# Optimization experiments

Measured on AMD Instinct MI355X. Metric: run time of the kernel, lower is better.

## Reference

```python
import jax, jax.numpy as jnp
from jax import lax
import numpy as np

B, CIN, H, W = 32, 256, 56, 56
BOTTLE, GROWTH = 128, 32
EPS = 1e-5
QMAX = 127.0  # 8-bit symmetric


def _fq(x, scale, qmax=QMAX):
    # fake-quantize with straight-through estimator
    q = jnp.clip(jnp.round(x / scale), -qmax - 1.0, qmax) * scale
    return x + lax.stop_gradient(q - x)


def fake_quant_act(x):
    # per-tensor symmetric 8-bit activation quantization (QuantAct)
    scale = lax.stop_gradient(jnp.max(jnp.abs(x)) / QMAX + 1e-8)
    return _fq(x, scale), scale


def quant_weight_pc(w):
    # per-output-channel symmetric 8-bit weight quantization, w: [O,I,kh,kw]
    scale = lax.stop_gradient(jnp.max(jnp.abs(w), axis=(1, 2, 3)) / QMAX + 1e-8)
    return _fq(w, scale[:, None, None, None]), scale


def conv2d(x, w, pad):
    return lax.conv_general_dilated(
        x, w, window_strides=(1, 1), padding=[(pad, pad), (pad, pad)],
        dimension_numbers=("NCHW", "OIHW", "NCHW"))


def setup_inputs() -> dict:
    key = jax.random.key(0)
    ks = jax.random.split(key, 12)
    return {
        "batch": jax.random.normal(ks[0], (B, CIN, H, W), jnp.float32),
        "input_scaling_factor": jnp.float32(0.05),
        "bn1_gamma": jax.random.uniform(ks[1], (CIN,), jnp.float32, 0.5, 1.5),
        "bn1_beta": jax.random.normal(ks[2], (CIN,), jnp.float32) * 0.1,
        "bn1_mean": jax.random.normal(ks[3], (CIN,), jnp.float32) * 0.1,
        "bn1_var": jax.random.uniform(ks[4], (CIN,), jnp.float32, 0.5, 1.5),
        "conv1_w": jax.random.normal(ks[5], (BOTTLE, CIN, 1, 1), jnp.float32) * 0.05,
        "bn2_gamma": jax.random.uniform(ks[6], (BOTTLE,), jnp.float32, 0.5, 1.5),
        "bn2_beta": jax.random.normal(ks[7], (BOTTLE,), jnp.float32) * 0.1,
        "bn2_mean": jax.random.normal(ks[8], (BOTTLE,), jnp.float32) * 0.1,
        "bn2_var": jax.random.uniform(ks[9], (BOTTLE,), jnp.float32, 0.5, 1.5),
        "conv2_w": jax.random.normal(ks[10], (GROWTH, BOTTLE, 3, 3), jnp.float32) * 0.05,
    }


def reference(batch, input_scaling_factor, bn1_gamma, bn1_beta, bn1_mean,
              bn1_var, conv1_w, bn2_gamma, bn2_beta, bn2_mean, bn2_var,
              conv2_w):
    s_in = input_scaling_factor
    # ---- QuantBn1: BN with fake-quantized folded weight/bias ----
    w1 = bn1_gamma * lax.rsqrt(bn1_var + EPS)            # [CIN]
    b1 = bn1_beta - bn1_mean * w1                        # [CIN]
    s_bn = lax.stop_gradient(jnp.max(jnp.abs(w1)) / QMAX + 1e-8)
    w1q = _fq(w1, s_bn)
    b1q = _fq(b1, s_in * s_bn, qmax=2.0 ** 31)           # bias quantized at s_in*s_w
    x = batch * w1q[None, :, None, None] + b1q[None, :, None, None]
    x = jax.nn.relu(x)                                   # act1
    x, s_a1 = fake_quant_act(x)                          # quant_act1
    # ---- QuantBnConv2d: fold bn2 into conv1 (1x1), per-channel weight quant ----
    t = bn2_gamma * lax.rsqrt(bn2_var + EPS)             # [BOTTLE]
    wf = conv1_w * t[:, None, None, None]
    bf = bn2_beta - bn2_mean * t
    wfq, s_w1 = quant_weight_pc(wf)                      # s_w1: [BOTTLE]
    bfq = _fq(bf, s_a1 * s_w1, qmax=2.0 ** 31)
    x = conv2d(x, wfq, pad=0) + bfq[None, :, None, None]
    x = jax.nn.relu(x)                                   # act2
    x, s_a2 = fake_quant_act(x)                          # quant_act2
    # ---- QuantConv2d: 3x3 growth conv, per-channel weight quant ----
    w2q, s_w2 = quant_weight_pc(conv2_w)
    x = conv2d(x, w2q, pad=1)                            # [B, GROWTH, H, W]
    # ---- concat + output requant ----
    cat = jnp.concatenate([batch, x], axis=1)            # [B, CIN+GROWTH, H, W]
    out, s_out = fake_quant_act(cat)                     # quant_act_output
    return out, s_out
```

## Files before the change

kernel.cpp:

```cpp
#include <hip/hip_runtime.h>

typedef __attribute__((ext_vector_type(8))) short bf16x8;
typedef __attribute__((ext_vector_type(4))) float f32x4;

constexpr int B_   = 32;
constexpr int CIN  = 256;
constexpr int HW   = 56 * 56;
constexpr int BOT  = 128;
constexpr int GRW  = 32;
constexpr int COUT = CIN + GRW;
constexpr int NBATCH = B_ * CIN * HW;
constexpr int NOUT   = B_ * COUT * HW;

constexpr int NSLOT = 32;
constexpr int SSTR  = 32;
constexpr int OFF_SLOT = 16;
constexpr int OFF_W1Q  = OFF_SLOT + 4 * NSLOT * SSTR;
constexpr int OFF_B1Q  = OFF_W1Q + 256;
constexpr int OFF_BFQ  = OFF_B1Q + 256;
constexpr int OFF_SC1  = OFF_BFQ + 128;
constexpr int OFF_SC2  = OFF_SC1 + 128;
constexpr int OFF_WQ1B = OFF_SC2 + 32;
constexpr int OFF_W2B  = OFF_WQ1B + 16384;
constexpr int OFF_END  = OFF_W2B + 18432;
constexpr size_t X2F_BYTE = (size_t)OFF_END * 4;
constexpr size_t X2F_FLTS = (size_t)B_ * 58 * 64 * 128;
constexpr size_t X3_BYTE  = X2F_BYTE + X2F_FLTS * 4;

__device__ __forceinline__ void slotAtomicMax(float* ws, int a, int s, float v) {
    atomicMax((unsigned*)ws + OFF_SLOT + a * NSLOT * SSTR + s * SSTR, __float_as_uint(v));
}
__device__ __forceinline__ float slotMax(const float* ws, int a) {
    float m = 0.0f;
    #pragma unroll
    for (int s = 0; s < NSLOT; s++)
        m = fmaxf(m, ws[OFF_SLOT + a * NSLOT * SSTR + s * SSTR]);
    return m;
}

__device__ __forceinline__ float blockReduceMax256(float v) {
    #pragma unroll
    for (int o = 32; o > 0; o >>= 1) v = fmaxf(v, __shfl_down(v, o, 64));
    __shared__ float sm[4];
    if ((threadIdx.x & 63) == 0) sm[threadIdx.x >> 6] = v;
    __syncthreads();
    return fmaxf(fmaxf(sm[0], sm[1]), fmaxf(sm[2], sm[3]));
}
__device__ __forceinline__ float waveReduceMax(float v) {
    #pragma unroll
    for (int o = 32; o > 0; o >>= 1) v = fmaxf(v, __shfl_down(v, o, 64));
    return v;
}
__device__ __forceinline__ float clamp8(float r)   { return fminf(fmaxf(r, -128.0f), 127.0f); }
__device__ __forceinline__ float clampBig(float r) { return fminf(fmaxf(r, -2147483648.0f), 2147483648.0f); }
__device__ __forceinline__ unsigned short bf16u(float f) { return (unsigned short)(__float_as_uint(f) >> 16); }

__global__ __launch_bounds__(256) void prep_kernel(const float* __restrict__ g1, const float* __restrict__ b1p,
                                                   const float* __restrict__ m1, const float* __restrict__ v1,
                                                   const float* __restrict__ s_in_p, float* __restrict__ ws) {
    int t = threadIdx.x;
    if (blockIdx.x == 0) {
        int c = t;
        unsigned* scal = (unsigned*)ws;
        for (int s = c; s < OFF_W1Q; s += 256) scal[s] = 0u;
        float s_in = *s_in_p;
        float r = 1.0f / sqrtf(v1[c] + 1e-5f);
        float w1 = __fmul_rn(g1[c], r);
        float b1 = __fsub_rn(b1p[c], __fmul_rn(m1[c], w1));
        float mx = blockReduceMax256(fabsf(w1));
        float s_bn = mx / 127.0f + 1e-8f;
        ws[OFF_W1Q + c] = __fmul_rn(clamp8(rintf(w1 / s_bn)), s_bn);
        float sb = __fmul_rn(s_in, s_bn);
        ws[OFF_B1Q + c] = __fmul_rn(clampBig(rintf(b1 / sb)), sb);
        return;
    }
    int b = blockIdx.x - 1;
    float4* x2f4 = (float4*)((char*)ws + X2F_BYTE);
    float4 z; z.x = z.y = z.z = z.w = 0.0f;
    for (int i = t; i < 2 * 58 * 32; i += 256) {
        int row  = i / (58 * 32);
        int rest = i - row * (58 * 32);
        int slot = rest >> 5, q = rest & 31;
        int hp = row ? 57 : 0;
        x2f4[(((size_t)(b * 58 + hp) * 64 + slot) * 128 >> 2) + q] = z;
    }
    for (int i = t; i < 56 * 2 * 32; i += 256) {
        int hp   = 1 + (i >> 6);
        int rest = i & 63;
        int slot = (rest >> 5) ? 57 : 0;
        int q = rest & 31;
        x2f4[(((size_t)(b * 58 + hp) * 64 + slot) * 128 >> 2) + q] = z;
    }
}

__global__ __launch_bounds__(256) void max1_kernel(const float4* __restrict__ batch4,
                                                   float* __restrict__ ws) {
    const float* w1q = ws + OFF_W1Q;
    const float* b1q = ws + OFF_B1Q;
    int tid = blockIdx.x * 256 + threadIdx.x;
    int row = tid >> 4;
    int f   = tid & 15;
    int c   = row & 255;
    float w = w1q[c], b = b1q[c];
    const float4* p = batch4 + (size_t)row * 784 + f;
    float mx1 = 0.0f, mxb = 0.0f;
    #pragma unroll 7
    for (int k = 0; k < 49; k++) {
        float4 v = p[k * 16];
        float x0 = fmaxf(__fadd_rn(__fmul_rn(v.x, w), b), 0.0f);
        float x1 = fmaxf(__fadd_rn(__fmul_rn(v.y, w), b), 0.0f);
        float x2 = fmaxf(__fadd_rn(__fmul_rn(v.z, w), b), 0.0f);
        float x3 = fmaxf(__fadd_rn(__fmul_rn(v.w, w), b), 0.0f);
        mx1 = fmaxf(mx1, fmaxf(fmaxf(x0, x1), fmaxf(x2, x3)));
        mxb = fmaxf(mxb, fmaxf(fmaxf(fabsf(v.x), fabsf(v.y)), fmaxf(fabsf(v.z), fabsf(v.w))));
    }
    mx1 = blockReduceMax256(mx1);
    __syncthreads();
    mxb = blockReduceMax256(mxb);
    if (threadIdx.x == 0) {
        int s = blockIdx.x & (NSLOT - 1);
        slotAtomicMax(ws, 0, s, mx1);
        slotAtomicMax(ws, 1, s, mxb);
    }
}

__global__ void prep2_kernel(const float* __restrict__ c1w,
                             const float* __restrict__ g2, const float* __restrict__ b2,
                             const float* __restrict__ m2, const float* __restrict__ v2,
                             const float* __restrict__ c2w, float* __restrict__ ws) {
    int bi = blockIdx.x;
    int t = threadIdx.x;
    unsigned short* wq1b = (unsigned short*)(ws + OFF_WQ1B);
    unsigned short* w2b  = (unsigned short*)(ws + OFF_W2B);
    if (bi < BOT) {
        int o = bi;
        float tt = __fmul_rn(g2[o], 1.0f / sqrtf(v2[o] + 1e-5f));
        float wf = __fmul_rn(c1w[o * CIN + t], tt);
        float mx = blockReduceMax256(fabsf(wf));
        float s_w1 = mx / 127.0f + 1e-8f;
        float m = clamp8(rintf(wf / s_w1));
        wq1b[o * CIN + t] = bf16u(m);
        if (t == 0) {
            float s_a1 = slotMax(ws, 0) / 127.0f + 1e-8f;
            ws[OFF_SC1 + o] = __fmul_rn(s_a1, s_w1);
            float bf = __fsub_rn(b2[o], __fmul_rn(m2[o], tt));
            float sb = __fmul_rn(s_a1, s_w1);
            ws[OFF_BFQ + o] = __fmul_rn(clampBig(rintf(bf / sb)), sb);
        }
    } else {
        int g = bi - BOT;
        float mx = 0.0f;
        for (int s = t; s < BOT * 9; s += 256) mx = fmaxf(mx, fabsf(c2w[g * BOT * 9 + s]));
        mx = blockReduceMax256(mx);
        float s_w2 = mx / 127.0f + 1e-8f;
        for (int s = t; s < BOT * 9; s += 256) {
            int c = s / 9, tap = s - c * 9;
            float m = clamp8(rintf(c2w[g * BOT * 9 + s] / s_w2));
            w2b[(tap * GRW + g) * BOT + c] = bf16u(m);
        }
        if (t == 0) ws[OFF_SC2 + g] = s_w2;
    }
}

__global__ __launch_bounds__(256) void conv1_kernel(const float4* __restrict__ batch4,
                                                    float* __restrict__ ws) {
    __shared__ unsigned ls[128 * 33];
    __shared__ unsigned short lA[64 * 136];
    __shared__ unsigned short lW[128 * 136];
    __shared__ float wred[4];
    const unsigned short* wq1b = (const unsigned short*)(ws + OFF_WQ1B);
    const float* w1q = ws + OFF_W1Q;
    const float* b1q = ws + OFF_B1Q;
    const float* sc1 = ws + OFF_SC1;
    const float* bfq = ws + OFF_BFQ;
    float* x2f = (float*)((char*)ws + X2F_BYTE);
    float s_a1 = slotMax(ws, 0) / 127.0f + 1e-8f;
    int b = blockIdx.x / 49, hw0 = (blockIdx.x % 49) * 64;
    int t = threadIdx.x, lane = t & 63, wv = t >> 6;
    int quad = lane >> 4, l16 = lane & 15;
    int mhalf = wv & 1, nhalf = wv >> 1;
    int f = t & 15, cb = t >> 4;
    f32x4 acc[2][4];
    #pragma unroll
    for (int i = 0; i < 2; i++)
        #pragma unroll
        for (int j = 0; j < 4; j++) acc[i][j] = (f32x4){0.f, 0.f, 0.f, 0.f};

    for (int kc = 0; kc < 256; kc += 128) {
        __syncthreads();
        {
            #pragma unroll
            for (int j = 0; j < 8; j++) {
                int cl = cb + j * 16;
                int c  = kc + cl;
                float w = w1q[c], bb = b1q[c];
                float4 v = batch4[(size_t)(b * 256 + c) * 784 + (hw0 >> 2) + f];
                unsigned q0 = bf16u(clamp8(rintf(fmaxf(__fadd_rn(__fmul_rn(v.x, w), bb), 0.0f) / s_a1)));
                unsigned q1 = bf16u(clamp8(rintf(fmaxf(__fadd_rn(__fmul_rn(v.y, w), bb), 0.0f) / s_a1)));
                unsigned q2 = bf16u(clamp8(rintf(fmaxf(__fadd_rn(__fmul_rn(v.z, w), bb), 0.0f) / s_a1)));
                unsigned q3 = bf16u(clamp8(rintf(fmaxf(__fadd_rn(__fmul_rn(v.w, w), bb), 0.0f) / s_a1)));
                ls[cl * 33 + f * 2]     = q0 | (q1 << 16);
                ls[cl * 33 + f * 2 + 1] = q2 | (q3 << 16);
            }
        }
        {
            int cw = t & 7, oi = t >> 3;
            #pragma unroll
            for (int r = 0; r < 4; r++) {
                int o = oi + r * 32;
                uint4 p0 = *(const uint4*)(wq1b + o * 256 + kc + cw * 16);
                uint4 p1 = *(const uint4*)(wq1b + o * 256 + kc + cw * 16 + 8);
                *(uint4*)&lW[o * 136 + cw * 16] = p0;
                *(uint4*)&lW[o * 136 + cw * 16 + 8] = p1;
            }
        }
        __syncthreads();
        {
            #pragma unroll
            for (int k = 0; k < 4; k++) {
                int task = t + k * 256;
                int hw = task & 63, c8 = task >> 6;
                int base = (hw >> 2) * 2 + ((hw >> 1) & 1);
                int sh = (hw & 1) * 16;
                unsigned v0 = ls[(c8 * 8 + 0) * 33 + base] >> sh;
                unsigned v1 = ls[(c8 * 8 + 1) * 33 + base] >> sh;
                unsigned v2 = ls[(c8 * 8 + 2) * 33 + base] >> sh;
                unsigned v3 = ls[(c8 * 8 + 3) * 33 + base] >> sh;
                unsigned v4 = ls[(c8 * 8 + 4) * 33 + base] >> sh;
                unsigned v5 = ls[(c8 * 8 + 5) * 33 + base] >> sh;
                unsigned v6 = ls[(c8 * 8 + 6) * 33 + base] >> sh;
                unsigned v7 = ls[(c8 * 8 + 7) * 33 + base] >> sh;
                uint4 pk;
                pk.x = (v0 & 0xffffu) | (v1 << 16);
                pk.y = (v2 & 0xffffu) | (v3 << 16);
                pk.z = (v4 & 0xffffu) | (v5 << 16);
                pk.w = (v6 & 0xffffu) | (v7 << 16);
                *(uint4*)&lA[hw * 136 + c8 * 8] = pk;
            }
        }
        __syncthreads();
        #pragma unroll
        for (int ks = 0; ks < 4; ks++) {
            bf16x8 a0 = *(const bf16x8*)&lA[(mhalf * 32 + l16) * 136 + ks * 32 + quad * 8];
            bf16x8 a1 = *(const bf16x8*)&lA[(mhalf * 32 + 16 + l16) * 136 + ks * 32 + quad * 8];
            #pragma unroll
            for (int nt = 0; nt < 4; nt++) {
                bf16x8 bfr = *(const bf16x8*)&lW[(nhalf * 64 + nt * 16 + l16) * 136 + ks * 32 + quad * 8];
                acc[0][nt] = __builtin_amdgcn_mfma_f32_16x16x32_bf16(a0, bfr, acc[0][nt], 0, 0, 0);
                acc[1][nt] = __builtin_amdgcn_mfma_f32_16x16x32_bf16(a1, bfr, acc[1][nt], 0, 0, 0);
            }
        }
    }
    float mx = 0.0f;
    #pragma unroll
    for (int mt = 0; mt < 2; mt++) {
        int hwg = hw0 + mhalf * 32 + mt * 16 + quad * 4;
        int h = (int)(((unsigned)hwg * 9363u) >> 19);
        int w = hwg - h * 56;
        float* base0 = x2f + ((size_t)(b * 58 + h + 1) * 64 + (w + 1)) * 128;
        #pragma unroll
        for (int nt = 0; nt < 4; nt++) {
            int o = nhalf * 64 + nt * 16 + l16;
            float s = sc1[o], bb = bfq[o];
            float v0 = fmaxf(__fadd_rn(__fmul_rn(acc[mt][nt][0], s), bb), 0.0f);
            float v1 = fmaxf(__fadd_rn(__fmul_rn(acc[mt][nt][1], s), bb), 0.0f);
            float v2 = fmaxf(__fadd_rn(__fmul_rn(acc[mt][nt][2], s), bb), 0.0f);
            float v3 = fmaxf(__fadd_rn(__fmul_rn(acc[mt][nt][3], s), bb), 0.0f);
            mx = fmaxf(mx, fmaxf(fmaxf(v0, v1), fmaxf(v2, v3)));
            base0[o]       = v0;
            base0[o + 128] = v1;
            base0[o + 256] = v2;
            base0[o + 384] = v3;
        }
    }
    mx = waveReduceMax(mx);
    if (lane == 0) wred[wv] = mx;
    __syncthreads();
    if (t == 0) {
        float m = fmaxf(fmaxf(wred[0], wred[1]), fmaxf(wred[2], wred[3]));
        slotAtomicMax(ws, 2, blockIdx.x & (NSLOT - 1), m);
    }
}

__global__ __launch_bounds__(256) void conv2_kernel(float* __restrict__ ws) {
    __shared__ unsigned short xt[4 * 58 * 40];
    __shared__ unsigned short wt[9 * 32 * 40];
    __shared__ float wred[4];
    const float* x2f = (const float*)((char*)ws + X2F_BYTE);
    const unsigned short* w2b = (const unsigned short*)(ws + OFF_W2B);
    const float* sc2 = ws + OFF_SC2;
    float* x3 = (float*)((char*)ws + X3_BYTE);
    int b = blockIdx.x / 28, hg = blockIdx.x % 28;
    int t = threadIdx.x, lane = t & 63, wv = t >> 6;
    int quad = lane >> 4, l16 = lane & 15;
    int r = wv >> 1;
    int h = hg * 2 + r;
    int wq = wv & 1;
    int w0 = wq * 24;
    float s_a2 = slotMax(ws, 2) / 127.0f + 1e-8f;
    float rinv = 1.0f / s_a2;
    const float* src = x2f + (size_t)(b * 58 + hg * 2) * 64 * 128;

    f32x4 acc[2][2];
    #pragma unroll
    for (int i = 0; i < 2; i++) { acc[i][0] = (f32x4){0.f,0.f,0.f,0.f}; acc[i][1] = (f32x4){0.f,0.f,0.f,0.f}; }

    for (int cs = 0; cs < 4; cs++) {
        __syncthreads();
        for (int s = t; s < 1152; s += 256) {
            int gi = s >> 2, q = s & 3;
            *(uint4*)&wt[gi * 40 + q * 8] = *(const uint4*)(w2b + gi * 128 + cs * 32 + q * 8);
        }
        #pragma unroll
        for (int k = 0; k < 8; k++) {
            int idx = t + k * 256;
            if (idx < 1856) {
                int row = idx / 464;
                int rem = idx - row * 464;
                int slot = rem >> 3, c4 = rem & 7;
                f32x4 v = *(const f32x4*)(src + (size_t)(row * 64 + slot) * 128 + cs * 32 + c4 * 4);
                unsigned q0 = bf16u(clamp8(rintf(v[0] * rinv)));
                unsigned q1 = bf16u(clamp8(rintf(v[1] * rinv)));
                unsigned q2 = bf16u(clamp8(rintf(v[2] * rinv)));
                unsigned q3 = bf16u(clamp8(rintf(v[3] * rinv)));
                uint2 pk; pk.x = q0 | (q1 << 16); pk.y = q2 | (q3 << 16);
                *(uint2*)&xt[(row * 58 + slot) * 40 + c4 * 4] = pk;
            }
        }
        __syncthreads();
        #pragma unroll
        for (int tap = 0; tap < 9; tap++) {
            int dh = tap / 3, dw = tap % 3;
            bf16x8 b0 = *(const bf16x8*)&wt[(tap * 32 + l16) * 40 + quad * 8];
            bf16x8 b1 = *(const bf16x8*)&wt[(tap * 32 + 16 + l16) * 40 + quad * 8];
            #pragma unroll
            for (int mt = 0; mt < 2; mt++) {
                int slot = w0 + mt * 16 + l16 + dw;
                bf16x8 a = *(const bf16x8*)&xt[((r + dh) * 58 + slot) * 40 + quad * 8];
                acc[mt][0] = __builtin_amdgcn_mfma_f32_16x16x32_bf16(a, b0, acc[mt][0], 0, 0, 0);
                acc[mt][1] = __builtin_amdgcn_mfma_f32_16x16x32_bf16(a, b1, acc[mt][1], 0, 0, 0);
            }
        }
    }
    float mx = 0.0f;
    #pragma unroll
    for (int nt = 0; nt < 2; nt++) {
        int g = nt * 16 + l16;
        float s2 = __fmul_rn(s_a2, sc2[g]);
        #pragma unroll
        for (int mt = 0; mt < 2; mt++) {
            int wb = w0 + mt * 16 + quad * 4;
            if (wq == 0 || wb >= 32) {
                float4 v;
                v.x = __fmul_rn(acc[mt][nt][0], s2);
                v.y = __fmul_rn(acc[mt][nt][1], s2);
                v.z = __fmul_rn(acc[mt][nt][2], s2);
                v.w = __fmul_rn(acc[mt][nt][3], s2);
                mx = fmaxf(mx, fmaxf(fmaxf(fabsf(v.x), fabsf(v.y)), fmaxf(fabsf(v.z), fabsf(v.w))));
                *(float4*)&x3[(size_t)(b * GRW + g) * HW + h * 56 + wb] = v;
            }
        }
    }
    mx = waveReduceMax(mx);
    if (lane == 0) wred[wv] = mx;
    __syncthreads();
    if (t == 0) {
        float m = fmaxf(fmaxf(wred[0], wred[1]), fmaxf(wred[2], wred[3]));
        slotAtomicMax(ws, 3, blockIdx.x & (NSLOT - 1), m);
    }
}

__global__ __launch_bounds__(256) void outq_kernel(const float4* __restrict__ batch4,
                                                   const float* __restrict__ ws,
                                                   float* __restrict__ out) {
    const float4* x34 = (const float4*)((const char*)ws + X3_BYTE);
    float maxb = slotMax(ws, 1);
    float max3 = slotMax(ws, 3);
    float s_out = fmaxf(maxb, max3) / 127.0f + 1e-8f;
    float4* out4 = (float4*)out;
    int n4 = NOUT / 4;
    for (int i = blockIdx.x * blockDim.x + threadIdx.x; i < n4; i += gridDim.x * blockDim.x) {
        int chl = i / 784;
        int b = chl / COUT;
        int ch = chl - b * COUT;
        int hw4 = i - chl * 784;
        float4 v;
        if (ch < CIN) v = batch4[(b * CIN + ch) * 784 + hw4];
        else          v = x34[(b * GRW + (ch - CIN)) * 784 + hw4];
        float4 r;
        r.x = __fmul_rn(clamp8(rintf(v.x / s_out)), s_out);
        r.y = __fmul_rn(clamp8(rintf(v.y / s_out)), s_out);
        r.z = __fmul_rn(clamp8(rintf(v.z / s_out)), s_out);
        r.w = __fmul_rn(clamp8(rintf(v.w / s_out)), s_out);
        out4[i] = r;
    }
    if (blockIdx.x == 0 && threadIdx.x == 0) out[NOUT] = s_out;
}

extern "C" void kernel_launch(void* const* d_in, const int* in_sizes, int n_in,
                              void* d_out, int out_size, void* d_ws, size_t ws_size,
                              hipStream_t stream) {
    const float* batch = (const float*)d_in[0];
    const float* s_in  = (const float*)d_in[1];
    const float* g1    = (const float*)d_in[2];
    const float* b1    = (const float*)d_in[3];
    const float* m1    = (const float*)d_in[4];
    const float* v1    = (const float*)d_in[5];
    const float* c1w   = (const float*)d_in[6];
    const float* g2    = (const float*)d_in[7];
    const float* b2    = (const float*)d_in[8];
    const float* m2    = (const float*)d_in[9];
    const float* v2    = (const float*)d_in[10];
    const float* c2w   = (const float*)d_in[11];
    float* out = (float*)d_out;
    float* ws  = (float*)d_ws;

    hipLaunchKernelGGL(prep_kernel, dim3(33), dim3(256), 0, stream, g1, b1, m1, v1, s_in, ws);
    hipLaunchKernelGGL(max1_kernel, dim3(512), dim3(256), 0, stream, (const float4*)batch, ws);
    hipLaunchKernelGGL(prep2_kernel, dim3(160), dim3(256), 0, stream, c1w, g2, b2, m2, v2, c2w, ws);
    hipLaunchKernelGGL(conv1_kernel, dim3(32 * 49), dim3(256), 0, stream, (const float4*)batch, ws);
    hipLaunchKernelGGL(conv2_kernel, dim3(32 * 28), dim3(256), 0, stream, ws);
    hipLaunchKernelGGL(outq_kernel, dim3(4096), dim3(256), 0, stream, (const float4*)batch, ws, out);
}
```

Before: 346.3 us.

## Fuse all stages into one cooperative persistent kernel with grid syncs

Replaces six separate launches (prep, max1, prep2, conv1, conv2, outq) with one cooperative kernel of 512 persistent blocks. The stages are split by grid.sync and use grid-stride loops over the original tiles. The prep work and the padding zeroing are merged into one virtual-block stage. The aim is to remove launch gaps and the tail idle time between kernels. In exchange it limits occupancy to the cooperative grid size, pays for four grid-wide barriers, and holds all stages' state in one large shared-memory footprint. If the cooperative launch fails, it falls back to the old multi-kernel path.

```diff
diff --git a/kernel.cpp b/kernel.cpp
--- a/kernel.cpp
+++ b/kernel.cpp
@@ -1,4 +1,7 @@
 #include <hip/hip_runtime.h>
+#include <hip/hip_cooperative_groups.h>
+
+namespace cg = cooperative_groups;
 
 typedef __attribute__((ext_vector_type(8))) short bf16x8;
 typedef __attribute__((ext_vector_type(4))) float f32x4;
@@ -9,7 +12,6 @@
 constexpr int BOT  = 128;
 constexpr int GRW  = 32;
 constexpr int COUT = CIN + GRW;
-constexpr int NBATCH = B_ * CIN * HW;
 constexpr int NOUT   = B_ * COUT * HW;
 
 constexpr int NSLOT = 32;
@@ -37,7 +39,6 @@
         m = fmaxf(m, ws[OFF_SLOT + a * NSLOT * SSTR + s * SSTR]);
     return m;
 }
-
 __device__ __forceinline__ float blockReduceMax256(float v) {
     #pragma unroll
     for (int o = 32; o > 0; o >>= 1) v = fmaxf(v, __shfl_down(v, o, 64));
@@ -54,6 +55,335 @@
 __device__ __forceinline__ float clamp8(float r)   { return fminf(fmaxf(r, -128.0f), 127.0f); }
 __device__ __forceinline__ float clampBig(float r) { return fminf(fmaxf(r, -2147483648.0f), 2147483648.0f); }
 __device__ __forceinline__ unsigned short bf16u(float f) { return (unsigned short)(__float_as_uint(f) >> 16); }
+
+__global__ __launch_bounds__(256, 2) void fused_kernel(
+        const float4* __restrict__ batch4, const float* __restrict__ s_in_p,
+        const float* __restrict__ g1, const float* __restrict__ b1p,
+        const float* __restrict__ m1, const float* __restrict__ v1,
+        const float* __restrict__ c1w, const float* __restrict__ g2,
+        const float* __restrict__ b2, const float* __restrict__ m2,
+        const float* __restrict__ v2, const float* __restrict__ c2w,
+        float* __restrict__ ws, float* __restrict__ out) {
+    cg::grid_group grid = cg::this_grid();
+    __shared__ __align__(16) char smem[69120];
+    int bid = blockIdx.x, gdim = gridDim.x;
+    int t = threadIdx.x, lane = t & 63, wv = t >> 6;
+    int quad = lane >> 4, l16 = lane & 15;
+
+    {
+        unsigned short* wq1b = (unsigned short*)(ws + OFF_WQ1B);
+        unsigned short* w2b  = (unsigned short*)(ws + OFF_W2B);
+        for (int vb = bid; vb < 193; vb += gdim) {
+            if (vb == 0) {
+                unsigned* scal = (unsigned*)ws;
+                for (int s = t; s < OFF_W1Q; s += 256) scal[s] = 0u;
+                int c = t;
+                float s_in = *s_in_p;
+                float r = 1.0f / sqrtf(v1[c] + 1e-5f);
+                float w1 = __fmul_rn(g1[c], r);
+                float b1 = __fsub_rn(b1p[c], __fmul_rn(m1[c], w1));
+                float mx = blockReduceMax256(fabsf(w1));
+                float s_bn = mx / 127.0f + 1e-8f;
+                ws[OFF_W1Q + c] = __fmul_rn(clamp8(rintf(w1 / s_bn)), s_bn);
+                float sb = __fmul_rn(s_in, s_bn);
+                ws[OFF_B1Q + c] = __fmul_rn(clampBig(rintf(b1 / sb)), sb);
+            } else if (vb <= 32) {
+                int b = vb - 1;
+                float4* x2f4 = (float4*)((char*)ws + X2F_BYTE);
+                float4 z; z.x = z.y = z.z = z.w = 0.0f;
+                for (int i = t; i < 2 * 58 * 32; i += 256) {
+                    int row  = i / (58 * 32);
+                    int rest = i - row * (58 * 32);
+                    int slot = rest >> 5, q = rest & 31;
+                    int hp = row ? 57 : 0;
+                    x2f4[(((size_t)(b * 58 + hp) * 64 + slot) * 128 >> 2) + q] = z;
+                }
+                for (int i = t; i < 56 * 2 * 32; i += 256) {
+                    int hp   = 1 + (i >> 6);
+                    int rest = i & 63;
+                    int slot = (rest >> 5) ? 57 : 0;
+                    int q = rest & 31;
+                    x2f4[(((size_t)(b * 58 + hp) * 64 + slot) * 128 >> 2) + q] = z;
+                }
+            } else if (vb < 33 + BOT) {
+                int o = vb - 33;
+                float tt = __fmul_rn(g2[o], 1.0f / sqrtf(v2[o] + 1e-5f));
+                float wf = __fmul_rn(c1w[o * CIN + t], tt);
+                float mx = blockReduceMax256(fabsf(wf));
+                float s_w1 = mx / 127.0f + 1e-8f;
+                float m = clamp8(rintf(wf / s_w1));
+                wq1b[o * CIN + t] = bf16u(m);
+                if (t == 0) {
+                    ws[OFF_SC1 + o] = s_w1;
+                    ws[OFF_BFQ + o] = __fsub_rn(b2[o], __fmul_rn(m2[o], tt));
+                }
+            } else {
+                int g = vb - 33 - BOT;
+                float mx = 0.0f;
+                for (int s = t; s < BOT * 9; s += 256) mx = fmaxf(mx, fabsf(c2w[g * BOT * 9 + s]));
+                mx = blockReduceMax256(mx);
+                float s_w2 = mx / 127.0f + 1e-8f;
+                for (int s = t; s < BOT * 9; s += 256) {
+                    int c = s / 9, tap = s - c * 9;
+                    float m = clamp8(rintf(c2w[g * BOT * 9 + s] / s_w2));
+                    w2b[(tap * GRW + g) * BOT + c] = bf16u(m);
+                }
+                if (t == 0) ws[OFF_SC2 + g] = s_w2;
+            }
+            __syncthreads();
+        }
+    }
+    grid.sync();
+
+    {
+        const float* w1q = ws + OFF_W1Q;
+        const float* b1q = ws + OFF_B1Q;
+        float mx1 = 0.0f, mxb = 0.0f;
+        for (int vb = bid; vb < 512; vb += gdim) {
+            int tid = vb * 256 + t;
+            int row = tid >> 4;
+            int f   = tid & 15;
+            int c   = row & 255;
+            float w = w1q[c], b = b1q[c];
+            const float4* p = batch4 + (size_t)row * 784 + f;
+            #pragma unroll 7
+            for (int k = 0; k < 49; k++) {
+                float4 v = p[k * 16];
+                float x0 = fmaxf(__fadd_rn(__fmul_rn(v.x, w), b), 0.0f);
+                float x1 = fmaxf(__fadd_rn(__fmul_rn(v.y, w), b), 0.0f);
+                float x2 = fmaxf(__fadd_rn(__fmul_rn(v.z, w), b), 0.0f);
+                float x3 = fmaxf(__fadd_rn(__fmul_rn(v.w, w), b), 0.0f);
+                mx1 = fmaxf(mx1, fmaxf(fmaxf(x0, x1), fmaxf(x2, x3)));
+                mxb = fmaxf(mxb, fmaxf(fmaxf(fabsf(v.x), fabsf(v.y)), fmaxf(fabsf(v.z), fabsf(v.w))));
+            }
+        }
+        mx1 = blockReduceMax256(mx1);
+        __syncthreads();
+        mxb = blockReduceMax256(mxb);
+        if (t == 0) {
+            int s = bid & (NSLOT - 1);
+            slotAtomicMax(ws, 0, s, mx1);
+            slotAtomicMax(ws, 1, s, mxb);
+        }
+    }
+    grid.sync();
+
+    {
+        unsigned*       ls = (unsigned*)smem;
+        unsigned short* lA = (unsigned short*)(smem + 16896);
+        unsigned short* lW = (unsigned short*)(smem + 34304);
+        const unsigned short* wq1b = (const unsigned short*)(ws + OFF_WQ1B);
+        const float* w1q = ws + OFF_W1Q;
+        const float* b1q = ws + OFF_B1Q;
+        const float* sw1 = ws + OFF_SC1;
+        const float* bfr = ws + OFF_BFQ;
+        float* x2f = (float*)((char*)ws + X2F_BYTE);
+        float s_a1 = slotMax(ws, 0) / 127.0f + 1e-8f;
+        int mhalf = wv & 1, nhalf = wv >> 1;
+        int f = t & 15, cb = t >> 4;
+        float mxph = 0.0f;
+        for (int tile = bid; tile < 32 * 49; tile += gdim) {
+            int b = tile / 49, hw0 = (tile % 49) * 64;
+            f32x4 acc[2][4];
+            #pragma unroll
+            for (int i = 0; i < 2; i++)
+                #pragma unroll
+                for (int j = 0; j < 4; j++) acc[i][j] = (f32x4){0.f, 0.f, 0.f, 0.f};
+            for (int kc = 0; kc < 256; kc += 128) {
+                __syncthreads();
+                #pragma unroll
+                for (int j = 0; j < 8; j++) {
+                    int cl = cb + j * 16;
+                    int c  = kc + cl;
+                    float w = w1q[c], bb = b1q[c];
+                    float4 v = batch4[(size_t)(b * 256 + c) * 784 + (hw0 >> 2) + f];
+                    unsigned q0 = bf16u(clamp8(rintf(fmaxf(__fadd_rn(__fmul_rn(v.x, w), bb), 0.0f) / s_a1)));
+                    unsigned q1 = bf16u(clamp8(rintf(fmaxf(__fadd_rn(__fmul_rn(v.y, w), bb), 0.0f) / s_a1)));
+                    unsigned q2 = bf16u(clamp8(rintf(fmaxf(__fadd_rn(__fmul_rn(v.z, w), bb), 0.0f) / s_a1)));
+                    unsigned q3 = bf16u(clamp8(rintf(fmaxf(__fadd_rn(__fmul_rn(v.w, w), bb), 0.0f) / s_a1)));
+                    ls[cl * 33 + f * 2]     = q0 | (q1 << 16);
+                    ls[cl * 33 + f * 2 + 1] = q2 | (q3 << 16);
+                }
+                {
+                    int cw = t & 7, oi = t >> 3;
+                    #pragma unroll
+                    for (int r = 0; r < 4; r++) {
+                        int o = oi + r * 32;
+                        uint4 p0 = *(const uint4*)(wq1b + o * 256 + kc + cw * 16);
+                        uint4 p1 = *(const uint4*)(wq1b + o * 256 + kc + cw * 16 + 8);
+                        *(uint4*)&lW[o * 136 + cw * 16] = p0;
+                        *(uint4*)&lW[o * 136 + cw * 16 + 8] = p1;
+                    }
+                }
+                __syncthreads();
+                #pragma unroll
+                for (int k = 0; k < 4; k++) {
+                    int task = t + k * 256;
+                    int hw = task & 63, c8 = task >> 6;
+                    int base = (hw >> 2) * 2 + ((hw >> 1) & 1);
+                    int sh = (hw & 1) * 16;
+                    unsigned v0 = ls[(c8 * 8 + 0) * 33 + base] >> sh;
+                    unsigned v1 = ls[(c8 * 8 + 1) * 33 + base] >> sh;
+                    unsigned v2 = ls[(c8 * 8 + 2) * 33 + base] >> sh;
+                    unsigned v3 = ls[(c8 * 8 + 3) * 33 + base] >> sh;
+                    unsigned v4 = ls[(c8 * 8 + 4) * 33 + base] >> sh;
+                    unsigned v5 = ls[(c8 * 8 + 5) * 33 + base] >> sh;
+                    unsigned v6 = ls[(c8 * 8 + 6) * 33 + base] >> sh;
+                    unsigned v7 = ls[(c8 * 8 + 7) * 33 + base] >> sh;
+                    uint4 pk;
+                    pk.x = (v0 & 0xffffu) | (v1 << 16);
+                    pk.y = (v2 & 0xffffu) | (v3 << 16);
+                    pk.z = (v4 & 0xffffu) | (v5 << 16);
+                    pk.w = (v6 & 0xffffu) | (v7 << 16);
+                    *(uint4*)&lA[hw * 136 + c8 * 8] = pk;
+                }
+                __syncthreads();
+                #pragma unroll
+                for (int ks = 0; ks < 4; ks++) {
+                    bf16x8 a0 = *(const bf16x8*)&lA[(mhalf * 32 + l16) * 136 + ks * 32 + quad * 8];
+                    bf16x8 a1 = *(const bf16x8*)&lA[(mhalf * 32 + 16 + l16) * 136 + ks * 32 + quad * 8];
+                    #pragma unroll
+                    for (int nt = 0; nt < 4; nt++) {
+                        bf16x8 bw = *(const bf16x8*)&lW[(nhalf * 64 + nt * 16 + l16) * 136 + ks * 32 + quad * 8];
+                        acc[0][nt] = __builtin_amdgcn_mfma_f32_16x16x32_bf16(a0, bw, acc[0][nt], 0, 0, 0);
+                        acc[1][nt] = __builtin_amdgcn_mfma_f32_16x16x32_bf16(a1, bw, acc[1][nt], 0, 0, 0);
+                    }
+                }
+            }
+            #pragma unroll
+            for (int mt = 0; mt < 2; mt++) {
+                int hwg = hw0 + mhalf * 32 + mt * 16 + quad * 4;
+                int h = (int)(((unsigned)hwg * 9363u) >> 19);
+                int w = hwg - h * 56;
+                float* base0 = x2f + ((size_t)(b * 58 + h + 1) * 64 + (w + 1)) * 128;
+                #pragma unroll
+                for (int nt = 0; nt < 4; nt++) {
+                    int o = nhalf * 64 + nt * 16 + l16;
+                    float s  = __fmul_rn(s_a1, sw1[o]);
+                    float bb = __fmul_rn(clampBig(rintf(bfr[o] / s)), s);
+                    float v0 = fmaxf(__fadd_rn(__fmul_rn(acc[mt][nt][0], s), bb), 0.0f);
+                    float v1 = fmaxf(__fadd_rn(__fmul_rn(acc[mt][nt][1], s), bb), 0.0f);
+                    float v2 = fmaxf(__fadd_rn(__fmul_rn(acc[mt][nt][2], s), bb), 0.0f);
+                    float v3 = fmaxf(__fadd_rn(__fmul_rn(acc[mt][nt][3], s), bb), 0.0f);
+                    mxph = fmaxf(mxph, fmaxf(fmaxf(v0, v1), fmaxf(v2, v3)));
+                    base0[o]       = v0;
+                    base0[o + 128] = v1;
+                    base0[o + 256] = v2;
+                    base0[o + 384] = v3;
+                }
+            }
+        }
+        float m = blockReduceMax256(mxph);
+        if (t == 0) slotAtomicMax(ws, 2, bid & (NSLOT - 1), m);
+    }
+    grid.sync();
+
+    {
+        unsigned short* xt = (unsigned short*)smem;
+        unsigned short* wt = (unsigned short*)(smem + 18560);
+        const float* x2f = (const float*)((char*)ws + X2F_BYTE);
+        const unsigned short* w2b = (const unsigned short*)(ws + OFF_W2B);
+        const float* sc2 = ws + OFF_SC2;
+        float* x3 = (float*)((char*)ws + X3_BYTE);
+        float s_a2 = slotMax(ws, 2) / 127.0f + 1e-8f;
+        float rinv = 1.0f / s_a2;
+        int r = wv >> 1;
+        int wq = wv & 1;
+        int w0 = wq * 24;
+        float mxph = 0.0f;
+        for (int tile = bid; tile < 32 * 28; tile += gdim) {
+            int b = tile / 28, hg = tile % 28;
+            int h = hg * 2 + r;
+            const float* src = x2f + (size_t)(b * 58 + hg * 2) * 64 * 128;
+            f32x4 acc[2][2];
+            #pragma unroll
+            for (int i = 0; i < 2; i++) { acc[i][0] = (f32x4){0.f,0.f,0.f,0.f}; acc[i][1] = (f32x4){0.f,0.f,0.f,0.f}; }
+            for (int cs = 0; cs < 4; cs++) {
+                __syncthreads();
+                for (int s = t; s < 1152; s += 256) {
+                    int gi = s >> 2, q = s & 3;
+                    *(uint4*)&wt[gi * 40 + q * 8] = *(const uint4*)(w2b + gi * 128 + cs * 32 + q * 8);
+                }
+                #pragma unroll
+                for (int k = 0; k < 8; k++) {
+                    int idx = t + k * 256;
+                    if (idx < 1856) {
+                        int row = idx / 464;
+                        int rem = idx - row * 464;
+                        int slot = rem >> 3, c4 = rem & 7;
+                        f32x4 v = *(const f32x4*)(src + (size_t)(row * 64 + slot) * 128 + cs * 32 + c4 * 4);
+                        unsigned q0 = bf16u(clamp8(rintf(v[0] * rinv)));
+                        unsigned q1 = bf16u(clamp8(rintf(v[1] * rinv)));
+                        unsigned q2 = bf16u(clamp8(rintf(v[2] * rinv)));
+                        unsigned q3 = bf16u(clamp8(rintf(v[3] * rinv)));
+                        uint2 pk; pk.x = q0 | (q1 << 16); pk.y = q2 | (q3 << 16);
+                        *(uint2*)&xt[(row * 58 + slot) * 40 + c4 * 4] = pk;
+                    }
+                }
+                __syncthreads();
+                #pragma unroll
+                for (int tap = 0; tap < 9; tap++) {
+                    int dh = tap / 3, dw = tap % 3;
+                    bf16x8 b0 = *(const bf16x8*)&wt[(tap * 32 + l16) * 40 + quad * 8];
+                    bf16x8 b1 = *(const bf16x8*)&wt[(tap * 32 + 16 + l16) * 40 + quad * 8];
+                    #pragma unroll
+                    for (int mt = 0; mt < 2; mt++) {
+                        int slot = w0 + mt * 16 + l16 + dw;
+                        bf16x8 a = *(const bf16x8*)&xt[((r + dh) * 58 + slot) * 40 + quad * 8];
+                        acc[mt][0] = __builtin_amdgcn_mfma_f32_16x16x32_bf16(a, b0, acc[mt][0], 0, 0, 0);
+                        acc[mt][1] = __builtin_amdgcn_mfma_f32_16x16x32_bf16(a, b1, acc[mt][1], 0, 0, 0);
+                    }
+                }
+            }
+            #pragma unroll
+            for (int nt = 0; nt < 2; nt++) {
+                int g = nt * 16 + l16;
+                float s2 = __fmul_rn(s_a2, sc2[g]);
+                #pragma unroll
+                for (int mt = 0; mt < 2; mt++) {
+                    int wb = w0 + mt * 16 + quad * 4;
+                    if (wq == 0 || wb >= 32) {
+                        float4 v;
+                        v.x = __fmul_rn(acc[mt][nt][0], s2);
+                        v.y = __fmul_rn(acc[mt][nt][1], s2);
+                        v.z = __fmul_rn(acc[mt][nt][2], s2);
+                        v.w = __fmul_rn(acc[mt][nt][3], s2);
+                        mxph = fmaxf(mxph, fmaxf(fmaxf(fabsf(v.x), fabsf(v.y)), fmaxf(fabsf(v.z), fabsf(v.w))));
+                        *(float4*)&x3[(size_t)(b * GRW + g) * HW + h * 56 + wb] = v;
+                    }
+                }
+            }
+        }
+        float m = blockReduceMax256(mxph);
+        if (t == 0) slotAtomicMax(ws, 3, bid & (NSLOT - 1), m);
+    }
+    grid.sync();
+
+    {
+        const float4* x34 = (const float4*)((const char*)ws + X3_BYTE);
+        float maxb = slotMax(ws, 1);
+        float max3 = slotMax(ws, 3);
+        float s_out = fmaxf(maxb, max3) / 127.0f + 1e-8f;
+        float4* out4 = (float4*)out;
+        int n4 = NOUT / 4;
+        for (int i = bid * 256 + t; i < n4; i += gdim * 256) {
+            int chl = i / 784;
+            int b = chl / COUT;
+            int ch = chl - b * COUT;
+            int hw4 = i - chl * 784;
+            float4 v;
+            if (ch < CIN) v = batch4[(b * CIN + ch) * 784 + hw4];
+            else          v = x34[(b * GRW + (ch - CIN)) * 784 + hw4];
+            float4 rr;
+            rr.x = __fmul_rn(clamp8(rintf(v.x / s_out)), s_out);
+            rr.y = __fmul_rn(clamp8(rintf(v.y / s_out)), s_out);
+            rr.z = __fmul_rn(clamp8(rintf(v.z / s_out)), s_out);
+            rr.w = __fmul_rn(clamp8(rintf(v.w / s_out)), s_out);
+            out4[i] = rr;
+        }
+        if (bid == 0 && t == 0) out[NOUT] = s_out;
+    }
+}
 
 __global__ __launch_bounds__(256) void prep_kernel(const float* __restrict__ g1, const float* __restrict__ b1p,
                                                    const float* __restrict__ m1, const float* __restrict__ v1,
@@ -188,20 +518,18 @@
 
     for (int kc = 0; kc < 256; kc += 128) {
         __syncthreads();
-        {
-            #pragma unroll
-            for (int j = 0; j < 8; j++) {
-                int cl = cb + j * 16;
-                int c  = kc + cl;
-                float w = w1q[c], bb = b1q[c];
-                float4 v = batch4[(size_t)(b * 256 + c) * 784 + (hw0 >> 2) + f];
-                unsigned q0 = bf16u(clamp8(rintf(fmaxf(__fadd_rn(__fmul_rn(v.x, w), bb), 0.0f) / s_a1)));
-                unsigned q1 = bf16u(clamp8(rintf(fmaxf(__fadd_rn(__fmul_rn(v.y, w), bb), 0.0f) / s_a1)));
-                unsigned q2 = bf16u(clamp8(rintf(fmaxf(__fadd_rn(__fmul_rn(v.z, w), bb), 0.0f) / s_a1)));
-                unsigned q3 = bf16u(clamp8(rintf(fmaxf(__fadd_rn(__fmul_rn(v.w, w), bb), 0.0f) / s_a1)));
-                ls[cl * 33 + f * 2]     = q0 | (q1 << 16);
-                ls[cl * 33 + f * 2 + 1] = q2 | (q3 << 16);
-            }
+        #pragma unroll
+        for (int j = 0; j < 8; j++) {
+            int cl = cb + j * 16;
+            int c  = kc + cl;
+            float w = w1q[c], bb = b1q[c];
+            float4 v = batch4[(size_t)(b * 256 + c) * 784 + (hw0 >> 2) + f];
+            unsigned q0 = bf16u(clamp8(rintf(fmaxf(__fadd_rn(__fmul_rn(v.x, w), bb), 0.0f) / s_a1)));
+            unsigned q1 = bf16u(clamp8(rintf(fmaxf(__fadd_rn(__fmul_rn(v.y, w), bb), 0.0f) / s_a1)));
+            unsigned q2 = bf16u(clamp8(rintf(fmaxf(__fadd_rn(__fmul_rn(v.z, w), bb), 0.0f) / s_a1)));
+            unsigned q3 = bf16u(clamp8(rintf(fmaxf(__fadd_rn(__fmul_rn(v.w, w), bb), 0.0f) / s_a1)));
+            ls[cl * 33 + f * 2]     = q0 | (q1 << 16);
+            ls[cl * 33 + f * 2 + 1] = q2 | (q3 << 16);
         }
         {
             int cw = t & 7, oi = t >> 3;
@@ -215,28 +543,26 @@
             }
         }
         __syncthreads();
-        {
-            #pragma unroll
-            for (int k = 0; k < 4; k++) {
-                int task = t + k * 256;
-                int hw = task & 63, c8 = task >> 6;
-                int base = (hw >> 2) * 2 + ((hw >> 1) & 1);
-                int sh = (hw & 1) * 16;
-                unsigned v0 = ls[(c8 * 8 + 0) * 33 + base] >> sh;
-                unsigned v1 = ls[(c8 * 8 + 1) * 33 + base] >> sh;
-                unsigned v2 = ls[(c8 * 8 + 2) * 33 + base] >> sh;
-                unsigned v3 = ls[(c8 * 8 + 3) * 33 + base] >> sh;
-                unsigned v4 = ls[(c8 * 8 + 4) * 33 + base] >> sh;
-                unsigned v5 = ls[(c8 * 8 + 5) * 33 + base] >> sh;
-                unsigned v6 = ls[(c8 * 8 + 6) * 33 + base] >> sh;
-                unsigned v7 = ls[(c8 * 8 + 7) * 33 + base] >> sh;
-                uint4 pk;
-                pk.x = (v0 & 0xffffu) | (v1 << 16);
-                pk.y = (v2 & 0xffffu) | (v3 << 16);
-                pk.z = (v4 & 0xffffu) | (v5 << 16);
-                pk.w = (v6 & 0xffffu) | (v7 << 16);
-                *(uint4*)&lA[hw * 136 + c8 * 8] = pk;
-            }
+        #pragma unroll
+        for (int k = 0; k < 4; k++) {
+            int task = t + k * 256;
+            int hw = task & 63, c8 = task >> 6;
+            int base = (hw >> 2) * 2 + ((hw >> 1) & 1);
+            int sh = (hw & 1) * 16;
+            unsigned v0 = ls[(c8 * 8 + 0) * 33 + base] >> sh;
+            unsigned v1 = ls[(c8 * 8 + 1) * 33 + base] >> sh;
+            unsigned v2 = ls[(c8 * 8 + 2) * 33 + base] >> sh;
+            unsigned v3 = ls[(c8 * 8 + 3) * 33 + base] >> sh;
+            unsigned v4 = ls[(c8 * 8 + 4) * 33 + base] >> sh;
+            unsigned v5 = ls[(c8 * 8 + 5) * 33 + base] >> sh;
+            unsigned v6 = ls[(c8 * 8 + 6) * 33 + base] >> sh;
+            unsigned v7 = ls[(c8 * 8 + 7) * 33 + base] >> sh;
+            uint4 pk;
+            pk.x = (v0 & 0xffffu) | (v1 << 16);
+            pk.y = (v2 & 0xffffu) | (v3 << 16);
+            pk.z = (v4 & 0xffffu) | (v5 << 16);
+            pk.w = (v6 & 0xffffu) | (v7 << 16);
+            *(uint4*)&lA[hw * 136 + c8 * 8] = pk;
         }
         __syncthreads();
         #pragma unroll
@@ -245,9 +571,9 @@
             bf16x8 a1 = *(const bf16x8*)&lA[(mhalf * 32 + 16 + l16) * 136 + ks * 32 + quad * 8];
             #pragma unroll
             for (int nt = 0; nt < 4; nt++) {
-                bf16x8 bfr = *(const bf16x8*)&lW[(nhalf * 64 + nt * 16 + l16) * 136 + ks * 32 + quad * 8];
-                acc[0][nt] = __builtin_amdgcn_mfma_f32_16x16x32_bf16(a0, bfr, acc[0][nt], 0, 0, 0);
-                acc[1][nt] = __builtin_amdgcn_mfma_f32_16x16x32_bf16(a1, bfr, acc[1][nt], 0, 0, 0);
+                bf16x8 bw = *(const bf16x8*)&lW[(nhalf * 64 + nt * 16 + l16) * 136 + ks * 32 + quad * 8];
+                acc[0][nt] = __builtin_amdgcn_mfma_f32_16x16x32_bf16(a0, bw, acc[0][nt], 0, 0, 0);
+                acc[1][nt] = __builtin_amdgcn_mfma_f32_16x16x32_bf16(a1, bw, acc[1][nt], 0, 0, 0);
             }
         }
     }
@@ -400,7 +726,7 @@
 extern "C" void kernel_launch(void* const* d_in, const int* in_sizes, int n_in,
                               void* d_out, int out_size, void* d_ws, size_t ws_size,
                               hipStream_t stream) {
-    const float* batch = (const float*)d_in[0];
+    const float4* batch = (const float4*)d_in[0];
     const float* s_in  = (const float*)d_in[1];
     const float* g1    = (const float*)d_in[2];
     const float* b1    = (const float*)d_in[3];
@@ -415,10 +741,23 @@
     float* out = (float*)d_out;
     float* ws  = (float*)d_ws;
 
-    hipLaunchKernelGGL(prep_kernel, dim3(33), dim3(256), 0, stream, g1, b1, m1, v1, s_in, ws);
-    hipLaunchKernelGGL(max1_kernel, dim3(512), dim3(256), 0, stream, (const float4*)batch, ws);
-    hipLaunchKernelGGL(prep2_kernel, dim3(160), dim3(256), 0, stream, c1w, g2, b2, m2, v2, c2w, ws);
-    hipLaunchKernelGGL(conv1_kernel, dim3(32 * 49), dim3(256), 0, stream, (const float4*)batch, ws);
-    hipLaunchKernelGGL(conv2_kernel, dim3(32 * 28), dim3(256), 0, stream, ws);
-    hipLaunchKernelGGL(outq_kernel, dim3(4096), dim3(256), 0, stream, (const float4*)batch, ws, out);
-}
+    void* args[] = {(void*)&batch, (void*)&s_in, (void*)&g1, (void*)&b1, (void*)&m1,
+                    (void*)&v1, (void*)&c1w, (void*)&g2, (void*)&b2, (void*)&m2,
+                    (void*)&v2, (void*)&c2w, (void*)&ws, (void*)&out};
+    hipError_t err = hipLaunchCooperativeKernel((const void*)fused_kernel, dim3(512), dim3(256),
+                                                args, 0, stream);
+    if (err != hipSuccess) {
+        (void)hipGetLastError();
+        err = hipLaunchCooperativeKernel((const void*)fused_kernel, dim3(256), dim3(256),
+                                         args, 0, stream);
+    }
+    if (err != hipSuccess) {
+        (void)hipGetLastError();
+        hipLaunchKernelGGL(prep_kernel, dim3(33), dim3(256), 0, stream, g1, b1, m1, v1, s_in, ws);
+        hipLaunchKernelGGL(max1_kernel, dim3(512), dim3(256), 0, stream, (const float4*)batch, ws);
+        hipLaunchKernelGGL(prep2_kernel, dim3(160), dim3(256), 0, stream, c1w, g2, b2, m2, v2, c2w, ws);
+        hipLaunchKernelGGL(conv1_kernel, dim3(32 * 49), dim3(256), 0, stream, (const float4*)batch, ws);
+        hipLaunchKernelGGL(conv2_kernel, dim3(32 * 28), dim3(256), 0, stream, ws);
+        hipLaunchKernelGGL(outq_kernel, dim3(4096), dim3(256), 0, stream, (const float4*)batch, ws, out);
+    }
+}
```

New measurement: 588.7 us. +70.0%, slower.
